# Performance work log

Hardware: AMD Instinct MI355X
Metric: run time of the kernel (lower is better)

## Reference

```python
import jax, jax.numpy as jnp
import numpy as np
import math

SL, BS, D, NH, PF, STRIDE, LAYERS = 2048, 4, 512, 8, 3, 1, 1
DH = D // NH
N_SPF = 9  # 0-2: hidden (a,t,v cross-attend to raw inputs); 3-5: cross (at,tv,va, shared for reverse dir); 6-8: self
EMBED_SCALE = math.sqrt(D)


def _ln(x, g, b):
    m = x.mean(-1, keepdims=True)
    var = ((x - m) ** 2).mean(-1, keepdims=True)
    return (x - m) / jnp.sqrt(var + 1e-5) * g + b


def _sinusoid(sl, d):
    half = d // 2
    inv = jnp.exp(jnp.arange(half, dtype=jnp.float32) * (-math.log(10000.0) / (half - 1)))
    ang = jnp.arange(sl, dtype=jnp.float32)[:, None] * inv[None, :]
    return jnp.concatenate([jnp.sin(ang), jnp.cos(ang)], axis=-1)  # (sl, d)


def setup_inputs() -> dict:
    key = jax.random.key(0)
    ks = jax.random.split(key, 16)
    s = 0.02
    p = {}
    p['a'] = jax.random.normal(ks[0], (SL, BS, D), jnp.float32)
    p['t'] = jax.random.normal(ks[1], (SL, BS, D), jnp.float32)
    p['v'] = jax.random.normal(ks[2], (SL, BS, D), jnp.float32)
    p['init_hiddens'] = s * jax.random.normal(ks[3], (3, D), jnp.float32)
    # stacked MultiheadAttention weights for the 9 SPF blocks
    p['wq'] = s * jax.random.normal(ks[4], (N_SPF, D, D), jnp.float32)
    p['bq'] = jnp.zeros((N_SPF, D), jnp.float32)
    p['wk'] = s * jax.random.normal(ks[5], (N_SPF, D, D), jnp.float32)
    p['bk'] = jnp.zeros((N_SPF, D), jnp.float32)
    p['wv'] = s * jax.random.normal(ks[6], (N_SPF, D, D), jnp.float32)
    p['bv'] = jnp.zeros((N_SPF, D), jnp.float32)
    p['wo'] = s * jax.random.normal(ks[7], (N_SPF, D, D), jnp.float32)
    p['bo'] = jnp.zeros((N_SPF, D), jnp.float32)
    p['ln_g'] = jnp.ones((N_SPF, D), jnp.float32)
    p['ln_b'] = jnp.zeros((N_SPF, D), jnp.float32)
    p['lnkv_g'] = jnp.ones((N_SPF, D), jnp.float32)
    p['lnkv_b'] = jnp.zeros((N_SPF, D), jnp.float32)
    # stacked FFN weights for the 9 FFN blocks
    p['w1'] = s * jax.random.normal(ks[8], (N_SPF, 4 * D, D), jnp.float32)
    p['b1'] = jnp.zeros((N_SPF, 4 * D), jnp.float32)
    p['w2'] = s * jax.random.normal(ks[9], (N_SPF, D, 4 * D), jnp.float32)
    p['b2'] = jnp.zeros((N_SPF, D), jnp.float32)
    p['fln_g'] = jnp.ones((N_SPF, D), jnp.float32)
    p['fln_b'] = jnp.zeros((N_SPF, D), jnp.float32)
    p['out_g'] = jnp.ones((D,), jnp.float32)
    p['out_b'] = jnp.zeros((D,), jnp.float32)
    return p


def reference(a, t, v, init_hiddens, wq, bq, wk, bk, wv, bv, wo, bo,
              ln_g, ln_b, lnkv_g, lnkv_b, w1, b1, w2, b2, fln_g, fln_b,
              out_g, out_b):
    scale = DH ** -0.5
    # precomputed strided modulo gather indices: r[i,j] = (i+1)*stride - pf + j
    idx = ((jnp.arange(SL) + 1) * STRIDE - PF)[:, None] + jnp.arange(PF)[None, :]  # (SL, PF)

    def spf(i, x, ctx, has_kv):
        # x: (SL, BS, D); ctx: (CL, BS, D) or None (self-attention on normed x)
        res = x
        xn = _ln(x, ln_g[i], ln_b[i])
        c = xn if ctx is None else ctx
        kv = c[idx % c.shape[0]]                      # (SL, PF, BS, D) modulo-gathered window
        if has_kv:
            kv = _ln(kv, lnkv_g[i], lnkv_b[i])
        q = (xn @ wq[i].T + bq[i]).reshape(SL, BS, NH, DH) * scale
        k = (kv @ wk[i].T + bk[i]).reshape(SL, PF, BS, NH, DH)
        vv = (kv @ wv[i].T + bv[i]).reshape(SL, PF, BS, NH, DH)
        attn = jax.nn.softmax(jnp.einsum('sbnd,spbnd->sbnp', q, k), axis=-1)
        o = jnp.einsum('sbnp,spbnd->sbnd', attn, vv).reshape(SL, BS, D)
        return res + o @ wo[i].T + bo[i]

    def ffn(i, x):
        h = jax.nn.relu(_ln(x, fln_g[i], fln_b[i]) @ w1[i].T + b1[i])
        return x + h @ w2[i].T + b2[i]

    pos = _sinusoid(SL, D)[:, None, :]
    a = a * EMBED_SCALE + pos
    t = t * EMBED_SCALE + pos
    v = v * EMBED_SCALE + pos
    h_a = jnp.broadcast_to(init_hiddens[0], (SL, BS, D))
    h_t = jnp.broadcast_to(init_hiddens[1], (SL, BS, D))
    h_v = jnp.broadcast_to(init_hiddens[2], (SL, BS, D))

    for _ in range(LAYERS):
        # hidden layer: hiddens cross-attend to raw modality streams
        h_a = ffn(0, spf(0, h_a, a, True))
        h_t = ffn(1, spf(1, h_t, t, True))
        h_v = ffn(2, spf(2, h_v, v, True))
        # cross layer: six branches, three shared weight sets (forward/reverse)
        h_at = ffn(3, spf(3, h_a, h_t, True))
        h_tv = ffn(4, spf(4, h_t, h_v, True))
        h_va = ffn(5, spf(5, h_v, h_a, True))
        h_ta = ffn(3, spf(3, h_t, h_a, True))
        h_vt = ffn(4, spf(4, h_v, h_t, True))
        h_av = ffn(5, spf(5, h_a, h_v, True))
        h_a, h_t, h_v = h_at + h_av, h_ta + h_tv, h_va + h_vt
        # self layer
        h_a = ffn(6, spf(6, h_a, None, False))
        h_t = ffn(7, spf(7, h_t, None, False))
        h_v = ffn(8, spf(8, h_v, None, False))

    return jnp.stack([_ln(h_a, out_g, out_b), _ln(h_t, out_g, out_b), _ln(h_v, out_g, out_b)])
```

## Files before the change

### kernel.cpp

```cpp
#include <hip/hip_runtime.h>

#define SL 2048
#define BS 4
#define DM 512
#define NH 8
#define DH 64
#define RD 8192
#define DF 2048
#define BK 32

typedef unsigned short u16;
typedef __attribute__((ext_vector_type(8))) short short8;
typedef __attribute__((ext_vector_type(4))) float f32x4;

__device__ __forceinline__ float bf2f(u16 u) {
  return __uint_as_float(((unsigned)u) << 16);
}
__device__ __forceinline__ u16 f2bf(float f) {
  unsigned u = __float_as_uint(f);
  unsigned r = (u + 0x7fffu + ((u >> 16) & 1u)) >> 16;
  return (u16)r;
}

typedef __attribute__((address_space(3))) unsigned int lds_u32;
typedef __attribute__((address_space(1))) unsigned int gbl_u32;
__device__ __forceinline__ void gload_lds16(const void* g, void* l) {
  __builtin_amdgcn_global_load_lds((gbl_u32*)g, (lds_u32*)l, 16, 0, 0);
}

struct GemmDesc {
  const u16* A;
  const u16* B;
  const float* bias;
  const float* res;
  u16* Cb;
  float* Cf;
  int K;
  int ldb;
  int nx;
  int ldc;
  int col0;
  int relu;
  int accum;
};
struct GemmBatch { GemmDesc d[9]; };

struct LnDesc {
  const float* x;
  const float* raw;
  const float* pos;
  const float* g; const float* b;
  u16* yb; float* yf;
};
struct LnBatch { LnDesc d[6]; };

struct AttnDesc { const u16* PK; u16* O; };
struct AttnBatch { AttnDesc d[3]; };

struct CvtDesc { const float* src; u16* dst; int n8; };
struct CvtBatch { CvtDesc d[3]; };

template<int TBN>
__global__ __launch_bounds__(256) void gemm_k(GemmBatch args) {
  constexpr int NFR = TBN / 32;
  constexpr int BU = TBN / 64;
  const GemmDesc g = args.d[blockIdx.z];
  __shared__ u16 As[2][128 * BK];
  __shared__ u16 Bs[2][TBN * BK];
  const int gX = gridDim.x;
  const int nwg = gX << 6;
  const int orig = blockIdx.y * gX + blockIdx.x;
  const int swz = (orig & 7) * (nwg >> 3) + (orig >> 3);
  const int by = swz / gX;
  const int bx = swz - by * gX;
  if (bx >= g.nx) return;
  const int K = g.K;
  const int ldb = g.ldb;
  const int t = threadIdx.x;
  const int w = t >> 6, l = t & 63;
  const u16* Ag = g.A + (size_t)by * 128 * K;
  const u16* Bg = g.B + (size_t)bx * TBN * ldb;
  f32x4 acc[4][NFR];
#pragma unroll
  for (int m = 0; m < 4; ++m)
#pragma unroll
    for (int n = 0; n < NFR; ++n) acc[m][n] = f32x4{0.f, 0.f, 0.f, 0.f};
  const int wr = (w >> 1) * 64;
  const int wc = (w & 1) * (TBN / 2);
  const int lr = l & 15;
  const int cxo = ((l >> 4) ^ ((l >> 1) & 3)) << 3;

  auto stage = [&](int buf, int k0) {
#pragma unroll
    for (int i = 0; i < 2; ++i) {
      const int u = (i << 8) + t;
      const int row = u >> 2;
      const int c = (u & 3) ^ ((row >> 1) & 3);
      gload_lds16(Ag + (size_t)row * K + k0 + (c << 3),
                  (char*)&As[buf][0] + (i << 12) + (w << 10));
    }
#pragma unroll
    for (int i = 0; i < BU; ++i) {
      const int u = (i << 8) + t;
      const int row = u >> 2;
      const int c = (u & 3) ^ ((row >> 1) & 3);
      gload_lds16(Bg + (size_t)row * ldb + k0 + (c << 3),
                  (char*)&Bs[buf][0] + (i << 12) + (w << 10));
    }
  };

  stage(0, 0);
  const int nt = K / BK;
  int cur = 0;
  for (int it = 0; it < nt; ++it) {
    __syncthreads();
    if (it + 1 < nt) stage(cur ^ 1, (it + 1) * BK);
    const u16* Ab = &As[cur][0];
    const u16* Bb = &Bs[cur][0];
    short8 af[4], bfr[NFR];
#pragma unroll
    for (int m = 0; m < 4; ++m)
      af[m] = *(const short8*)(Ab + (wr + m * 16 + lr) * BK + cxo);
#pragma unroll
    for (int n = 0; n < NFR; ++n)
      bfr[n] = *(const short8*)(Bb + (wc + n * 16 + lr) * BK + cxo);
#pragma unroll
    for (int m = 0; m < 4; ++m)
#pragma unroll
      for (int n = 0; n < NFR; ++n)
        acc[m][n] = __builtin_amdgcn_mfma_f32_16x16x32_bf16(af[m], bfr[n], acc[m][n], 0, 0, 0);
    cur ^= 1;
  }

  const int c0 = bx * TBN + wc + lr;
  const int r0 = by * 128 + wr + ((l >> 4) << 2);
#pragma unroll
  for (int n = 0; n < NFR; ++n) {
    const int gc = c0 + n * 16;
    const float bi = g.bias ? g.bias[gc] : 0.f;
#pragma unroll
    for (int m = 0; m < 4; ++m) {
#pragma unroll
      for (int r = 0; r < 4; ++r) {
        const size_t off = (size_t)(r0 + m * 16 + r) * g.ldc + g.col0 + gc;
        float v = acc[m][n][r] + bi;
        if (g.res) v += g.res[off];
        if (g.relu) v = fmaxf(v, 0.f);
        if (g.Cb) {
          g.Cb[off] = f2bf(v);
        } else {
          if (g.accum) v += g.Cf[off];
          g.Cf[off] = v;
        }
      }
    }
  }
}

__global__ __launch_bounds__(256) void ln_k(LnBatch args) {
  LnDesc d = args.d[blockIdx.y];
  const int row = blockIdx.x * 4 + (threadIdx.x >> 6);
  const int l = threadIdx.x & 63;
  float xv[8];
  if (d.raw) {
    const float* rp = d.raw + (size_t)row * DM + l * 8;
    const float* pp = d.pos + (size_t)(row >> 2) * DM + l * 8;
    float4 r0 = *(const float4*)rp, r1 = *(const float4*)(rp + 4);
    float4 p0 = *(const float4*)pp, p1 = *(const float4*)(pp + 4);
    const float SC = 22.627416998f;
    xv[0] = r0.x * SC + p0.x; xv[1] = r0.y * SC + p0.y;
    xv[2] = r0.z * SC + p0.z; xv[3] = r0.w * SC + p0.w;
    xv[4] = r1.x * SC + p1.x; xv[5] = r1.y * SC + p1.y;
    xv[6] = r1.z * SC + p1.z; xv[7] = r1.w * SC + p1.w;
  } else {
    const float* xp = d.x + (size_t)row * DM + l * 8;
    float4 x0 = *(const float4*)xp, x1 = *(const float4*)(xp + 4);
    xv[0] = x0.x; xv[1] = x0.y; xv[2] = x0.z; xv[3] = x0.w;
    xv[4] = x1.x; xv[5] = x1.y; xv[6] = x1.z; xv[7] = x1.w;
  }
  float s = 0.f, ss = 0.f;
#pragma unroll
  for (int j = 0; j < 8; ++j) { s += xv[j]; ss += xv[j] * xv[j]; }
#pragma unroll
  for (int m = 1; m < 64; m <<= 1) {
    s += __shfl_xor(s, m, 64);
    ss += __shfl_xor(ss, m, 64);
  }
  const float mean = s * (1.f / DM);
  const float var = ss * (1.f / DM) - mean * mean;
  const float rstd = rsqrtf(var + 1e-5f);
  float4 g0 = *(const float4*)(d.g + l * 8);
  float4 g1 = *(const float4*)(d.g + l * 8 + 4);
  float4 b0 = *(const float4*)(d.b + l * 8);
  float4 b1 = *(const float4*)(d.b + l * 8 + 4);
  float gv[8] = {g0.x, g0.y, g0.z, g0.w, g1.x, g1.y, g1.z, g1.w};
  float bv[8] = {b0.x, b0.y, b0.z, b0.w, b1.x, b1.y, b1.z, b1.w};
  float y[8];
#pragma unroll
  for (int j = 0; j < 8; ++j) y[j] = (xv[j] - mean) * rstd * gv[j] + bv[j];
  if (d.yb) {
    short8 p;
#pragma unroll
    for (int j = 0; j < 8; ++j) p[j] = (short)f2bf(y[j]);
    *(short8*)(d.yb + (size_t)row * DM + l * 8) = p;
  } else {
    float* o = d.yf + (size_t)row * DM + l * 8;
    *(float4*)o = float4{y[0], y[1], y[2], y[3]};
    *(float4*)(o + 4) = float4{y[4], y[5], y[6], y[7]};
  }
}

__global__ __launch_bounds__(256) void attn_k(AttnBatch args) {
  AttnDesc d = args.d[blockIdx.y];
  const int idx = blockIdx.x * 256 + threadIdx.x;
  const int h = idx & 7;
  const int b = (idx >> 3) & 3;
  const int s = idx >> 5;
  const int s0 = (s + SL - 2) & (SL - 1);
  const int s1 = (s + SL - 1) & (SL - 1);
  const size_t bq_ = (size_t)(s * BS + b) * 1536 + h * DH;
  const size_t b0 = (size_t)(s0 * BS + b) * 1536 + h * DH;
  const size_t b1 = (size_t)(s1 * BS + b) * 1536 + h * DH;
  float d0 = 0.f, d1 = 0.f, d2 = 0.f;
#pragma unroll
  for (int c = 0; c < 8; ++c) {
    short8 q8 = *(const short8*)(d.PK + bq_ + c * 8);
    short8 k0 = *(const short8*)(d.PK + b0 + 512 + c * 8);
    short8 k1 = *(const short8*)(d.PK + b1 + 512 + c * 8);
    short8 k2 = *(const short8*)(d.PK + bq_ + 512 + c * 8);
#pragma unroll
    for (int e = 0; e < 8; ++e) {
      const float q = bf2f((u16)q8[e]);
      d0 += q * bf2f((u16)k0[e]);
      d1 += q * bf2f((u16)k1[e]);
      d2 += q * bf2f((u16)k2[e]);
    }
  }
  const float mx = fmaxf(d0, fmaxf(d1, d2));
  float e0 = expf(d0 - mx), e1 = expf(d1 - mx), e2 = expf(d2 - mx);
  const float inv = 1.f / (e0 + e1 + e2);
  e0 *= inv; e1 *= inv; e2 *= inv;
  const size_t ro = (size_t)(s * BS + b) * DM + h * DH;
#pragma unroll
  for (int c = 0; c < 8; ++c) {
    short8 v0 = *(const short8*)(d.PK + b0 + 1024 + c * 8);
    short8 v1 = *(const short8*)(d.PK + b1 + 1024 + c * 8);
    short8 v2 = *(const short8*)(d.PK + bq_ + 1024 + c * 8);
    short8 o8;
#pragma unroll
    for (int e = 0; e < 8; ++e)
      o8[e] = (short)f2bf(e0 * bf2f((u16)v0[e]) + e1 * bf2f((u16)v1[e]) + e2 * bf2f((u16)v2[e]));
    *(short8*)(d.O + ro + c * 8) = o8;
  }
}

__global__ __launch_bounds__(256) void packqkv_k(const float* wq, const float* wk,
                                                 const float* wv, u16* dst) {
  const int i = blockIdx.x * 256 + threadIdx.x;
  const int br = i / 98304;
  const int r = i - br * 98304;
  const int sec = r / 32768;
  const int r2 = r - sec * 32768;
  const float* src = (sec == 0) ? wq : (sec == 1) ? wk : wv;
  const float* sp = src + (size_t)br * 262144 + (size_t)r2 * 8;
  const float sc = (sec == 0) ? 0.125f : 1.f;
  short8 o;
#pragma unroll
  for (int e = 0; e < 8; ++e) o[e] = (short)f2bf(sp[e] * sc);
  *(short8*)(dst + (size_t)br * 786432 + (size_t)sec * 262144 + (size_t)r2 * 8) = o;
}

__global__ __launch_bounds__(256) void packbias_k(const float* bq, const float* bk,
                                                  const float* bv, float* dst) {
  const int i = blockIdx.x * 256 + threadIdx.x;
  if (i >= 13824) return;
  const int br = i / 1536;
  const int r = i - br * 1536;
  const int sec = r >> 9;
  const int j = r & 511;
  float v = (sec == 0) ? bq[br * 512 + j] * 0.125f
          : (sec == 1) ? bk[br * 512 + j] : bv[br * 512 + j];
  dst[i] = v;
}

__global__ __launch_bounds__(256) void cvt_k(CvtBatch a) {
  CvtDesc d = a.d[blockIdx.y];
  const int stride = gridDim.x * 256;
  for (int i = blockIdx.x * 256 + threadIdx.x; i < d.n8; i += stride) {
    float4 x0 = ((const float4*)d.src)[i * 2];
    float4 x1 = ((const float4*)d.src)[i * 2 + 1];
    short8 r;
    r[0] = (short)f2bf(x0.x); r[1] = (short)f2bf(x0.y);
    r[2] = (short)f2bf(x0.z); r[3] = (short)f2bf(x0.w);
    r[4] = (short)f2bf(x1.x); r[5] = (short)f2bf(x1.y);
    r[6] = (short)f2bf(x1.z); r[7] = (short)f2bf(x1.w);
    *(short8*)(d.dst + (size_t)i * 8) = r;
  }
}

__global__ __launch_bounds__(256) void pos_k(float* pos) {
  const int i = blockIdx.x * 256 + threadIdx.x;
  const int dd = i & (DM - 1);
  const int s = i >> 9;
  const int j = (dd < 256) ? dd : dd - 256;
  const float inv = expf((float)j * -0.036119374f);
  const float ang = (float)s * inv;
  pos[i] = (dd < 256) ? sinf(ang) : cosf(ang);
}

__global__ __launch_bounds__(256) void hinit_k(const float* init, float* H) {
  const int z = blockIdx.y;
  const int i = blockIdx.x * 256 + threadIdx.x;
  float4 w = ((const float4*)(init + z * DM))[i & 127];
  ((float4*)(H + (size_t)z * RD * DM))[i] = w;
}

extern "C" void kernel_launch(void* const* d_in, const int* in_sizes, int n_in,
                              void* d_out, int out_size, void* d_ws, size_t ws_size,
                              hipStream_t stream) {
  (void)in_sizes; (void)n_in; (void)out_size;
  const float* in_a  = (const float*)d_in[0];
  const float* in_t  = (const float*)d_in[1];
  const float* in_v  = (const float*)d_in[2];
  const float* initH = (const float*)d_in[3];
  const float* wq = (const float*)d_in[4];
  const float* bq = (const float*)d_in[5];
  const float* wk = (const float*)d_in[6];
  const float* bk = (const float*)d_in[7];
  const float* wv = (const float*)d_in[8];
  const float* bv = (const float*)d_in[9];
  const float* wo = (const float*)d_in[10];
  const float* bo = (const float*)d_in[11];
  const float* ln_g = (const float*)d_in[12];
  const float* ln_b = (const float*)d_in[13];
  const float* lnkv_g = (const float*)d_in[14];
  const float* lnkv_b = (const float*)d_in[15];
  const float* w1 = (const float*)d_in[16];
  const float* b1 = (const float*)d_in[17];
  const float* w2 = (const float*)d_in[18];
  const float* b2 = (const float*)d_in[19];
  const float* fln_g = (const float*)d_in[20];
  const float* fln_b = (const float*)d_in[21];
  const float* out_g = (const float*)d_in[22];
  const float* out_b = (const float*)d_in[23];
  float* out = (float*)d_out;

  char* ws = (char*)d_ws;
  const size_t slotF = (size_t)RD * DM * 4;
  const size_t slotB = (size_t)RD * DM * 2;
  u16* wqkv_b = (u16*)(ws);
  u16* wo_b   = (u16*)(ws + 14155776);
  u16* w1_b   = (u16*)(ws + 18874368);
  u16* w2_b   = (u16*)(ws + 37748736);
  float* bqkv = (float*)(ws + 56623104);
  const size_t oH = 56678400;
  float* Hs[3];  float* Acc[3];
  for (int j = 0; j < 3; ++j) Hs[j]  = (float*)(ws + oH + (size_t)j * slotF);
  for (int j = 0; j < 3; ++j) Acc[j] = out + (size_t)j * RD * DM;
  float* pos = (float*)(ws + oH + 3 * slotF);
  const size_t oL = oH + 3 * slotF + 4194304;
  const size_t laneSz = 5 * slotB;
  int G = 1;
  if (ws_size >= oL + 3 * laneSz) G = 3;
  else if (ws_size >= oL + 2 * laneSz) G = 2;

  auto PSLOT = [&](int j, int k) {
    return (u16*)(ws + oL + (size_t)j * laneSz + (size_t)k * slotB);
  };
  auto SOUT = [&](int j) { return (float*)PSLOT(j, 0); };

  packqkv_k<<<dim3(3456), 256, 0, stream>>>(wq, wk, wv, wqkv_b);
  packbias_k<<<dim3(54), 256, 0, stream>>>(bq, bk, bv, bqkv);
  {
    CvtBatch cb{};
    cb.d[0] = CvtDesc{wo, wo_b, 294912};
    cb.d[1] = CvtDesc{w1, w1_b, 1179648};
    cb.d[2] = CvtDesc{w2, w2_b, 1179648};
    cvt_k<<<dim3(1024, 3), 256, 0, stream>>>(cb);
  }
  pos_k<<<dim3(4096), 256, 0, stream>>>(pos);
  hinit_k<<<dim3(4096, 3), 256, 0, stream>>>(initH, (float*)(ws + oH));

  auto run_group = [&](int g, float* const* xv, float* const* ctx, const float* const* raw,
                       const int* wi, float* const* fout, int accum) {
    {
      LnBatch lb{}; int nd = 0;
      for (int j = 0; j < g; ++j)
        lb.d[nd++] = LnDesc{xv[j], nullptr, nullptr,
                            ln_g + wi[j] * DM, ln_b + wi[j] * DM, PSLOT(j, 3), nullptr};
      if (ctx || raw)
        for (int j = 0; j < g; ++j)
          lb.d[nd++] = LnDesc{ctx ? ctx[j] : nullptr, raw ? raw[j] : nullptr, pos,
                              lnkv_g + wi[j] * DM, lnkv_b + wi[j] * DM, PSLOT(j, 4), nullptr};
      ln_k<<<dim3(2048, nd), 256, 0, stream>>>(lb);
    }
    {
      GemmBatch gb{}; int nz = 0, gx;
      if (!ctx && !raw) {
        for (int j = 0; j < g; ++j)
          gb.d[nz++] = GemmDesc{PSLOT(j, 3), wqkv_b + (size_t)wi[j] * 786432,
                                bqkv + wi[j] * 1536, nullptr, PSLOT(j, 0), nullptr,
                                512, 512, 12, 1536, 0, 0, 0};
        gx = 12;
      } else {
        for (int j = 0; j < g; ++j) {
          gb.d[nz++] = GemmDesc{PSLOT(j, 3), wqkv_b + (size_t)wi[j] * 786432,
                                bqkv + wi[j] * 1536, nullptr, PSLOT(j, 0), nullptr,
                                512, 512, 4, 1536, 0, 0, 0};
          gb.d[nz++] = GemmDesc{PSLOT(j, 4), wqkv_b + (size_t)wi[j] * 786432 + 262144,
                                bqkv + wi[j] * 1536 + 512, nullptr, PSLOT(j, 0), nullptr,
                                512, 512, 8, 1536, 512, 0, 0};
        }
        gx = 8;
      }
      gemm_k<128><<<dim3(gx, 64, nz), 256, 0, stream>>>(gb);
    }
    {
      AttnBatch ab{};
      for (int j = 0; j < g; ++j) ab.d[j] = AttnDesc{PSLOT(j, 0), PSLOT(j, 3)};
      attn_k<<<dim3(256, g), 256, 0, stream>>>(ab);
    }
    {
      GemmBatch gb{};
      for (int j = 0; j < g; ++j)
        gb.d[j] = GemmDesc{PSLOT(j, 3), wo_b + (size_t)wi[j] * DM * DM, bo + wi[j] * DM,
                           xv[j], nullptr, SOUT(j), 512, 512, 8, 512, 0, 0, 0};
      gemm_k<64><<<dim3(8, 64, g), 256, 0, stream>>>(gb);
    }
    {
      LnBatch lb{};
      for (int j = 0; j < g; ++j)
        lb.d[j] = LnDesc{SOUT(j), nullptr, nullptr,
                         fln_g + wi[j] * DM, fln_b + wi[j] * DM, PSLOT(j, 4), nullptr};
      ln_k<<<dim3(2048, g), 256, 0, stream>>>(lb);
    }
    for (int h = 0; h < 2; ++h) {
      {
        GemmBatch gb{};
        for (int j = 0; j < g; ++j)
          gb.d[j] = GemmDesc{PSLOT(j, 4), w1_b + (size_t)wi[j] * DF * DM + (size_t)h * 524288,
                             b1 + wi[j] * DF + h * 1024, nullptr, PSLOT(j, 2), nullptr,
                             512, 512, 8, 1024, 0, 1, 0};
        gemm_k<128><<<dim3(8, 64, g), 256, 0, stream>>>(gb);
      }
      {
        GemmBatch gb{};
        for (int j = 0; j < g; ++j)
          gb.d[j] = GemmDesc{PSLOT(j, 2), w2_b + (size_t)wi[j] * DM * DF + (size_t)h * 1024,
                             h == 0 ? b2 + wi[j] * DM : nullptr,
                             h == 0 ? SOUT(j) : nullptr, nullptr, fout[j],
                             1024, 2048, 8, 512, 0, 0, h == 0 ? accum : 1};
        gemm_k<64><<<dim3(8, 64, g), 256, 0, stream>>>(gb);
      }
    }
  };

  auto drive = [&](int n, float* const* xv, float* const* ctx, const float* const* raw,
                   const int* wi, float* const* fout, int accum) {
    for (int b = 0; b < n; b += G) {
      const int g = (G < n - b) ? G : n - b;
      run_group(g, xv + b, ctx ? ctx + b : nullptr, raw ? raw + b : nullptr,
                wi + b, fout + b, accum);
    }
  };

  {
    float* xv[3] = {Hs[0], Hs[1], Hs[2]};
    const float* raw[3] = {in_a, in_t, in_v};
    const int wi[3] = {0, 1, 2};
    float* fout[3] = {Hs[0], Hs[1], Hs[2]};
    drive(3, xv, nullptr, raw, wi, fout, 0);
  }
  {
    float* xv[3] = {Hs[0], Hs[1], Hs[2]};
    float* ctx[3] = {Hs[1], Hs[2], Hs[0]};
    const int wi[3] = {3, 4, 5};
    float* fout[3] = {Acc[0], Acc[1], Acc[2]};
    drive(3, xv, ctx, nullptr, wi, fout, 0);
  }
  {
    float* xv[3] = {Hs[1], Hs[2], Hs[0]};
    float* ctx[3] = {Hs[0], Hs[1], Hs[2]};
    const int wi[3] = {3, 4, 5};
    float* fout[3] = {Acc[1], Acc[2], Acc[0]};
    drive(3, xv, ctx, nullptr, wi, fout, 1);
  }
  {
    float* xv[3] = {Acc[0], Acc[1], Acc[2]};
    const int wi[3] = {6, 7, 8};
    float* fout[3] = {Hs[0], Hs[1], Hs[2]};
    drive(3, xv, nullptr, nullptr, wi, fout, 0);
  }
  {
    LnBatch lb{};
    for (int j = 0; j < 3; ++j)
      lb.d[j] = LnDesc{Hs[j], nullptr, nullptr, out_g, out_b, nullptr,
                       out + (size_t)j * RD * DM};
    ln_k<<<dim3(2048, 3), 256, 0, stream>>>(lb);
  }
}
```

Before: 2.246 ms.

## Triple-buffer GEMM loads and stage epilogue through LDS for coalesced stores

Switches the GEMM main loop from double to triple buffering, using explicit vmcnt waits and split barriers so two tiles of global-to-LDS loads stay in flight. The epilogue now writes results into a swizzled LDS tile and then issues vectorized, coalesced global stores for bf16 outputs and for TBN=64 fp32 outputs with residual and accumulate. QKV projections are batched as three uniform 512-wide descriptors per branch. This adds LDS use, which may lower occupancy, and relies on hand-counted vmcnt values matching the number of loads issued.

Measured after the change: 2.257 ms. Within noise of the previous version (+0.5%).

```diff
diff --git a/kernel.cpp b/kernel.cpp
--- a/kernel.cpp
+++ b/kernel.cpp
@@ -27,6 +27,8 @@
 __device__ __forceinline__ void gload_lds16(const void* g, void* l) {
   __builtin_amdgcn_global_load_lds((gbl_u32*)g, (lds_u32*)l, 16, 0, 0);
 }
+
+#define VMCNT(n) asm volatile("s_waitcnt vmcnt(" #n ")" ::: "memory")
 
 struct GemmDesc {
   const u16* A;
@@ -64,9 +66,12 @@
 __global__ __launch_bounds__(256) void gemm_k(GemmBatch args) {
   constexpr int NFR = TBN / 32;
   constexpr int BU = TBN / 64;
+  constexpr int ABYTES = 128 * BK * 2;
+  constexpr int BBYTES = TBN * BK * 2;
+  constexpr int BUFB = ABYTES + BBYTES;
+  constexpr int LDSB = (3 * BUFB > 32768) ? 3 * BUFB : 32768;
+  __shared__ char lds[LDSB];
   const GemmDesc g = args.d[blockIdx.z];
-  __shared__ u16 As[2][128 * BK];
-  __shared__ u16 Bs[2][TBN * BK];
   const int gX = gridDim.x;
   const int nwg = gX << 6;
   const int orig = blockIdx.y * gX + blockIdx.x;
@@ -91,13 +96,13 @@
   const int cxo = ((l >> 4) ^ ((l >> 1) & 3)) << 3;
 
   auto stage = [&](int buf, int k0) {
+    char* base = lds + buf * BUFB;
 #pragma unroll
     for (int i = 0; i < 2; ++i) {
       const int u = (i << 8) + t;
       const int row = u >> 2;
       const int c = (u & 3) ^ ((row >> 1) & 3);
-      gload_lds16(Ag + (size_t)row * K + k0 + (c << 3),
-                  (char*)&As[buf][0] + (i << 12) + (w << 10));
+      gload_lds16(Ag + (size_t)row * K + k0 + (c << 3), base + (i << 12) + (w << 10));
     }
 #pragma unroll
     for (int i = 0; i < BU; ++i) {
@@ -105,18 +110,27 @@
       const int row = u >> 2;
       const int c = (u & 3) ^ ((row >> 1) & 3);
       gload_lds16(Bg + (size_t)row * ldb + k0 + (c << 3),
-                  (char*)&Bs[buf][0] + (i << 12) + (w << 10));
+                  base + ABYTES + (i << 12) + (w << 10));
     }
   };
 
+  const int nt = K / BK;
   stage(0, 0);
-  const int nt = K / BK;
-  int cur = 0;
+  if (nt > 1) stage(1, BK);
+  int bcur = 0;
   for (int it = 0; it < nt; ++it) {
-    __syncthreads();
-    if (it + 1 < nt) stage(cur ^ 1, (it + 1) * BK);
-    const u16* Ab = &As[cur][0];
-    const u16* Bb = &Bs[cur][0];
+    __builtin_amdgcn_s_barrier();
+    if (it + 2 < nt) {
+      int b2 = bcur + 2; if (b2 >= 3) b2 -= 3;
+      stage(b2, (it + 2) * BK);
+    }
+    if (it + 2 < nt)      { if constexpr (TBN == 128) VMCNT(8); else VMCNT(6); }
+    else if (it + 1 < nt) { if constexpr (TBN == 128) VMCNT(4); else VMCNT(3); }
+    else                  VMCNT(0);
+    __builtin_amdgcn_s_barrier();
+    asm volatile("" ::: "memory");
+    const u16* Ab = (const u16*)(lds + bcur * BUFB);
+    const u16* Bb = (const u16*)(lds + bcur * BUFB + ABYTES);
     short8 af[4], bfr[NFR];
 #pragma unroll
     for (int m = 0; m < 4; ++m)
@@ -129,30 +143,89 @@
 #pragma unroll
       for (int n = 0; n < NFR; ++n)
         acc[m][n] = __builtin_amdgcn_mfma_f32_16x16x32_bf16(af[m], bfr[n], acc[m][n], 0, 0, 0);
-    cur ^= 1;
-  }
-
-  const int c0 = bx * TBN + wc + lr;
-  const int r0 = by * 128 + wr + ((l >> 4) << 2);
-#pragma unroll
-  for (int n = 0; n < NFR; ++n) {
-    const int gc = c0 + n * 16;
-    const float bi = g.bias ? g.bias[gc] : 0.f;
-#pragma unroll
-    for (int m = 0; m < 4; ++m) {
-#pragma unroll
-      for (int r = 0; r < 4; ++r) {
-        const size_t off = (size_t)(r0 + m * 16 + r) * g.ldc + g.col0 + gc;
-        float v = acc[m][n][r] + bi;
-        if (g.res) v += g.res[off];
-        if (g.relu) v = fmaxf(v, 0.f);
-        if (g.Cb) {
-          g.Cb[off] = f2bf(v);
-        } else {
+    bcur = (bcur + 1 == 3) ? 0 : bcur + 1;
+  }
+  __syncthreads();
+
+  const int r0g = by * 128;
+  if (g.Cb) {
+    char* tile = lds;
+#pragma unroll
+    for (int n = 0; n < NFR; ++n) {
+      const int col = wc + n * 16 + lr;
+      const float bi = g.bias ? g.bias[bx * TBN + col] : 0.f;
+#pragma unroll
+      for (int m = 0; m < 4; ++m)
+#pragma unroll
+        for (int r = 0; r < 4; ++r) {
+          const int row = wr + m * 16 + ((l >> 4) << 2) + r;
+          float v = acc[m][n][r] + bi;
+          if (g.relu) v = fmaxf(v, 0.f);
+          const int off = row * (TBN * 2) + ((((col >> 3) ^ (row & 7))) << 4) + ((col & 7) << 1);
+          *(u16*)(tile + off) = f2bf(v);
+        }
+    }
+    __syncthreads();
+    constexpr int GR = TBN / 16;
+    const int row = t >> 1, half = t & 1;
+#pragma unroll
+    for (int j = 0; j < GR; ++j) {
+      const int ci = half * GR + j;
+      short8 v = *(const short8*)(tile + row * (TBN * 2) + ((ci ^ (row & 7)) << 4));
+      *(short8*)&g.Cb[(size_t)(r0g + row) * g.ldc + g.col0 + bx * TBN + ci * 8] = v;
+    }
+  } else if constexpr (TBN == 64) {
+    char* tile = lds;
+#pragma unroll
+    for (int n = 0; n < NFR; ++n) {
+      const int col = wc + n * 16 + lr;
+      const float bi = g.bias ? g.bias[bx * 64 + col] : 0.f;
+#pragma unroll
+      for (int m = 0; m < 4; ++m)
+#pragma unroll
+        for (int r = 0; r < 4; ++r) {
+          const int row = wr + m * 16 + ((l >> 4) << 2) + r;
+          float v = acc[m][n][r] + bi;
+          if (g.relu) v = fmaxf(v, 0.f);
+          const int off = row * 256 + (((col >> 2) ^ (row & 7)) << 4) + ((col & 3) << 2);
+          *(float*)(tile + off) = v;
+        }
+    }
+    __syncthreads();
+    const int row = t >> 1, half = t & 1;
+#pragma unroll
+    for (int j = 0; j < 8; ++j) {
+      const int ci = half * 8 + j;
+      float4 v = *(const float4*)(tile + row * 256 + ((ci ^ (row & 7)) << 4));
+      const size_t off = (size_t)(r0g + row) * g.ldc + g.col0 + bx * 64 + ci * 4;
+      if (g.res) {
+        float4 rr = *(const float4*)&g.res[off];
+        v.x += rr.x; v.y += rr.y; v.z += rr.z; v.w += rr.w;
+      }
+      if (g.accum) {
+        float4 rr = *(const float4*)&g.Cf[off];
+        v.x += rr.x; v.y += rr.y; v.z += rr.z; v.w += rr.w;
+      }
+      *(float4*)&g.Cf[off] = v;
+    }
+  } else {
+    const int c0 = bx * TBN + wc + lr;
+    const int r0 = r0g + wr + ((l >> 4) << 2);
+#pragma unroll
+    for (int n = 0; n < NFR; ++n) {
+      const int gc = c0 + n * 16;
+      const float bi = g.bias ? g.bias[gc - bx * TBN] : 0.f;
+#pragma unroll
+      for (int m = 0; m < 4; ++m)
+#pragma unroll
+        for (int r = 0; r < 4; ++r) {
+          const size_t off = (size_t)(r0 + m * 16 + r) * g.ldc + g.col0 + gc;
+          float v = acc[m][n][r] + bi;
+          if (g.res) v += g.res[off];
+          if (g.relu) v = fmaxf(v, 0.f);
           if (g.accum) v += g.Cf[off];
           g.Cf[off] = v;
         }
-      }
     }
   }
 }
@@ -395,25 +468,20 @@
       ln_k<<<dim3(2048, nd), 256, 0, stream>>>(lb);
     }
     {
-      GemmBatch gb{}; int nz = 0, gx;
-      if (!ctx && !raw) {
-        for (int j = 0; j < g; ++j)
-          gb.d[nz++] = GemmDesc{PSLOT(j, 3), wqkv_b + (size_t)wi[j] * 786432,
-                                bqkv + wi[j] * 1536, nullptr, PSLOT(j, 0), nullptr,
-                                512, 512, 12, 1536, 0, 0, 0};
-        gx = 12;
-      } else {
-        for (int j = 0; j < g; ++j) {
-          gb.d[nz++] = GemmDesc{PSLOT(j, 3), wqkv_b + (size_t)wi[j] * 786432,
-                                bqkv + wi[j] * 1536, nullptr, PSLOT(j, 0), nullptr,
-                                512, 512, 4, 1536, 0, 0, 0};
-          gb.d[nz++] = GemmDesc{PSLOT(j, 4), wqkv_b + (size_t)wi[j] * 786432 + 262144,
-                                bqkv + wi[j] * 1536 + 512, nullptr, PSLOT(j, 0), nullptr,
-                                512, 512, 8, 1536, 512, 0, 0};
+      GemmBatch gb{}; int nz = 0;
+      const bool self = (!ctx && !raw);
+      for (int j = 0; j < g; ++j) {
+        const u16* aq = PSLOT(j, 3);
+        const u16* akv = self ? PSLOT(j, 3) : PSLOT(j, 4);
+        for (int s = 0; s < 3; ++s) {
+          gb.d[nz++] = GemmDesc{s == 0 ? aq : akv,
+                                wqkv_b + (size_t)wi[j] * 786432 + (size_t)s * 262144,
+                                bqkv + wi[j] * 1536 + s * 512,
+                                nullptr, PSLOT(j, 0), nullptr,
+                                512, 512, 4, 1536, s * 512, 0, 0};
         }
-        gx = 8;
       }
-      gemm_k<128><<<dim3(gx, 64, nz), 256, 0, stream>>>(gb);
+      gemm_k<128><<<dim3(4, 64, nz), 256, 0, stream>>>(gb);
     }
     {
       AttnBatch ab{};
```
